# Kernel optimization log

Measured on AMD Instinct MI355X. Metric: run time of the kernel, lower is better.

Reference implementation:

```python
import jax, jax.numpy as jnp
import numpy as np

ORDER = 128


def setup_inputs() -> dict:
    key = jax.random.key(0)
    k1, k2 = jax.random.split(key)
    B, T, p, Tf = 16, 131072, ORDER, 8192
    excitation = jax.random.normal(k1, (B, T), dtype=jnp.float32)
    # reflection coefficients in (-1, 1)
    rc = jax.random.uniform(k2, (B, p, Tf), dtype=jnp.float32, minval=-1.0, maxval=1.0)
    return {"excitation": excitation, "rc": rc}


def _rc_to_lpc(rc):
    """Step-up (Levinson-Durbin) recursion: reflection coeffs -> LPC coeffs.

    rc: (B, p, T_f)  ->  a: (B, T_f, p+1) with a[..., 0] == 1.
    Each step i does a[..., 1:i+2] += k_i * flip(a[..., :i+1]).
    Implemented as a full-width masked gather so it runs in one lax.scan.
    """
    B, p, Tf = rc.shape
    ks = jnp.transpose(rc, (1, 0, 2))  # (p, B, Tf)
    a0 = jnp.zeros((B, Tf, p + 1), rc.dtype).at[..., 0].set(1.0)
    j = jnp.arange(p + 1)

    def step(a, inp):
        i, k = inp  # i: scalar order index, k: (B, Tf)
        src = jnp.clip(i + 1 - j, 0, p)
        a_rev = jnp.take(a, src, axis=-1)          # flipped prefix, full width
        mask = (j >= 1) & (j <= i + 1)             # only positions 1..i+1 update
        a = a + jnp.where(mask, k[..., None] * a_rev, jnp.zeros((), a.dtype))
        return a, None

    a, _ = jax.lax.scan(step, a0, (jnp.arange(p), ks))
    return a


def reference(excitation, rc):
    # forward: rc = rc * 0.98, then step-up recursion to LPC coefficients.
    # (the original module's FFT synthesis path is dead code and the audio
    #  passthrough is the identity; the live math is the recursion below)
    rc = rc * 0.98
    return _rc_to_lpc(rc)
```

## Files before the change

### kernel.cpp

```cpp
#include <hip/hip_runtime.h>


#define NB   16
#define ORD  128
#define TF   8192
#define PD   16

template<int M, int J>
struct PairUpd {
    static __device__ __forceinline__ void run(float (&a)[ORD + 1], float k) {
        const float lo = a[J];
        const float hi = a[M - J];
        a[J]     = fmaf(k, hi, lo);
        a[M - J] = fmaf(k, lo, hi);
        if constexpr (2 * (J + 1) < M) PairUpd<M, J + 1>::run(a, k);
    }
};

template<int M>
struct Step {
    static __device__ __forceinline__ void run(float (&a)[ORD + 1],
                                               float (&kq)[PD],
                                               const float* __restrict__ rcp) {
        constexpr int slot = (M - 1) & (PD - 1);
        const float k = 0.98f * kq[slot];
        if constexpr (M - 1 + PD < ORD)
            kq[slot] = rcp[(size_t)(M - 1 + PD) * TF];
        asm volatile("" ::: "memory");
        if constexpr (M > 2) PairUpd<M, 1>::run(a, k);
        if constexpr ((M & 1) == 0) {
            const float mid = a[M / 2];
            a[M / 2] = fmaf(k, mid, mid);
        }
        a[M] = k;
        if constexpr (M < ORD) Step<M + 1>::run(a, kq, rcp);
    }
};

template<int J>
struct Stage {
    static __device__ __forceinline__ void run(float* __restrict__ dst,
                                               const float (&a)[ORD + 1]) {
        dst[J] = a[J];
        if constexpr (J < ORD) Stage<J + 1>::run(dst, a);
    }
};

__global__ __launch_bounds__(256)
__attribute__((amdgpu_waves_per_eu(2, 2)))
void lpc_stepup_kernel(const float* __restrict__ rc, float* __restrict__ out) {
    const int tid = threadIdx.x;
    const int gid = blockIdx.x * 256 + tid;
    const int b = gid >> 13;
    const int t = gid & (TF - 1);
    const float* rcp = rc + ((size_t)b * ORD) * TF + t;

    float kq[PD];
#pragma unroll
    for (int i = 0; i < PD; ++i) kq[i] = rcp[(size_t)i * TF];

    float a[ORD + 1];
    a[0] = 1.0f;
    Step<1>::run(a, kq, rcp);

    __shared__ __align__(16) float lds[64 * (ORD + 1)];
    const int my_round = tid >> 6;
    const int row      = tid & 63;
    float* out_block = out + (size_t)blockIdx.x * 256 * (ORD + 1);

    for (int r = 0; r < 4; ++r) {
        __syncthreads();
        if (my_round == r)
            Stage<0>::run(&lds[row * (ORD + 1)], a);
        __syncthreads();
        const float4* lds4 = (const float4*)lds;
        float4* out4 = (float4*)(out_block + (size_t)r * 64 * (ORD + 1));
        for (int e = tid; e < (64 * (ORD + 1)) / 4; e += 256)
            out4[e] = lds4[e];
    }
}

extern "C" void kernel_launch(void* const* d_in, const int* in_sizes, int n_in,
                              void* d_out, int out_size, void* d_ws, size_t ws_size,
                              hipStream_t stream) {
    const float* rc = (const float*)d_in[1];
    float* out = (float*)d_out;
    dim3 grid((NB * TF) / 256);
    dim3 block(256);
    hipLaunchKernelGGL(lpc_stepup_kernel, grid, block, 0, stream, rc, out);
}
```

Before: 139.6 us.

## Use single-wave blocks and preload all reflection coefficients into registers

Each block now holds one 64-lane wave instead of four, so every wave stages its own 64 rows through LDS and writes them out without taking turns across four rounds. All 128 reflection coefficients are loaded into registers up front, replacing the rolling 16-deep prefetch queue that loaded inside the recursion. This removes the serialized staging rounds and the per-step loads, but raises register pressure (about 257 floats live) and restricts occupancy to one wave per EU, with little left to hide memory latency.

```diff
diff --git a/kernel.cpp b/kernel.cpp
--- a/kernel.cpp
+++ b/kernel.cpp
@@ -4,7 +4,6 @@
 #define NB   16
 #define ORD  128
 #define TF   8192
-#define PD   16
 
 template<int M, int J>
 struct PairUpd {
@@ -20,20 +19,15 @@
 template<int M>
 struct Step {
     static __device__ __forceinline__ void run(float (&a)[ORD + 1],
-                                               float (&kq)[PD],
-                                               const float* __restrict__ rcp) {
-        constexpr int slot = (M - 1) & (PD - 1);
-        const float k = 0.98f * kq[slot];
-        if constexpr (M - 1 + PD < ORD)
-            kq[slot] = rcp[(size_t)(M - 1 + PD) * TF];
-        asm volatile("" ::: "memory");
+                                               const float (&kq)[ORD]) {
+        const float k = 0.98f * kq[M - 1];
         if constexpr (M > 2) PairUpd<M, 1>::run(a, k);
         if constexpr ((M & 1) == 0) {
             const float mid = a[M / 2];
             a[M / 2] = fmaf(k, mid, mid);
         }
         a[M] = k;
-        if constexpr (M < ORD) Step<M + 1>::run(a, kq, rcp);
+        if constexpr (M < ORD) Step<M + 1>::run(a, kq);
     }
 };
 
@@ -46,38 +40,32 @@
     }
 };
 
-__global__ __launch_bounds__(256)
-__attribute__((amdgpu_waves_per_eu(2, 2)))
+__global__ __launch_bounds__(64)
+__attribute__((amdgpu_waves_per_eu(1, 1)))
 void lpc_stepup_kernel(const float* __restrict__ rc, float* __restrict__ out) {
-    const int tid = threadIdx.x;
-    const int gid = blockIdx.x * 256 + tid;
+    const int lane = threadIdx.x;
+    const int gid  = blockIdx.x * 64 + lane;
     const int b = gid >> 13;
     const int t = gid & (TF - 1);
     const float* rcp = rc + ((size_t)b * ORD) * TF + t;
 
-    float kq[PD];
+    float kq[ORD];
 #pragma unroll
-    for (int i = 0; i < PD; ++i) kq[i] = rcp[(size_t)i * TF];
+    for (int i = 0; i < ORD; ++i) kq[i] = rcp[(size_t)i * TF];
 
     float a[ORD + 1];
     a[0] = 1.0f;
-    Step<1>::run(a, kq, rcp);
+    Step<1>::run(a, kq);
 
     __shared__ __align__(16) float lds[64 * (ORD + 1)];
-    const int my_round = tid >> 6;
-    const int row      = tid & 63;
-    float* out_block = out + (size_t)blockIdx.x * 256 * (ORD + 1);
+    Stage<0>::run(&lds[lane * (ORD + 1)], a);
+    __syncthreads();
 
-    for (int r = 0; r < 4; ++r) {
-        __syncthreads();
-        if (my_round == r)
-            Stage<0>::run(&lds[row * (ORD + 1)], a);
-        __syncthreads();
-        const float4* lds4 = (const float4*)lds;
-        float4* out4 = (float4*)(out_block + (size_t)r * 64 * (ORD + 1));
-        for (int e = tid; e < (64 * (ORD + 1)) / 4; e += 256)
-            out4[e] = lds4[e];
-    }
+    const float4* lds4 = (const float4*)lds;
+    float4* out4 = (float4*)(out + (size_t)blockIdx.x * 64 * (ORD + 1));
+#pragma unroll 4
+    for (int e = lane; e < (64 * (ORD + 1)) / 4; e += 64)
+        out4[e] = lds4[e];
 }
 
 extern "C" void kernel_launch(void* const* d_in, const int* in_sizes, int n_in,
@@ -85,7 +73,7 @@
                               hipStream_t stream) {
     const float* rc = (const float*)d_in[1];
     float* out = (float*)d_out;
-    dim3 grid((NB * TF) / 256);
-    dim3 block(256);
+    dim3 grid((NB * TF) / 64);
+    dim3 block(64);
     hipLaunchKernelGGL(lpc_stepup_kernel, grid, block, 0, stream, rc, out);
 }
```

Result: slower. 144.2 us (+3.3%).

## Split step-up recursion into two kernels with prefix round-trip through output

Applied to the files above, without the earlier changes.

Splits the 128-step recursion into two launches. The first runs orders 1..52 and writes the partial coefficients straight to the output buffer. The second reloads them, loads the remaining reflection coefficients all up front, finishes the recursion, and writes the final rows through LDS using 128-thread blocks. This replaces the rolling 16-deep prefetch queue with fully preloaded k values in each phase, which may change register pressure and latency hiding. In exchange it adds an extra uncoalesced global write and read of 52 floats per column, plus a second launch.

```diff
diff --git a/kernel.cpp b/kernel.cpp
--- a/kernel.cpp
+++ b/kernel.cpp
@@ -1,10 +1,10 @@
 #include <hip/hip_runtime.h>
 
 
-#define NB   16
-#define ORD  128
-#define TF   8192
-#define PD   16
+#define NB    16
+#define ORD   128
+#define TF    8192
+#define SPLIT 52
 
 template<int M, int J>
 struct PairUpd {
@@ -17,23 +17,18 @@
     }
 };
 
-template<int M>
+template<int M, int MEND, int K0, int NK>
 struct Step {
     static __device__ __forceinline__ void run(float (&a)[ORD + 1],
-                                               float (&kq)[PD],
-                                               const float* __restrict__ rcp) {
-        constexpr int slot = (M - 1) & (PD - 1);
-        const float k = 0.98f * kq[slot];
-        if constexpr (M - 1 + PD < ORD)
-            kq[slot] = rcp[(size_t)(M - 1 + PD) * TF];
-        asm volatile("" ::: "memory");
+                                               const float (&kq)[NK]) {
+        const float k = 0.98f * kq[M - 1 - K0];
         if constexpr (M > 2) PairUpd<M, 1>::run(a, k);
         if constexpr ((M & 1) == 0) {
             const float mid = a[M / 2];
             a[M / 2] = fmaf(k, mid, mid);
         }
         a[M] = k;
-        if constexpr (M < ORD) Step<M + 1>::run(a, kq, rcp);
+        if constexpr (M < MEND) Step<M + 1, MEND, K0, NK>::run(a, kq);
     }
 };
 
@@ -48,34 +43,62 @@
 
 __global__ __launch_bounds__(256)
 __attribute__((amdgpu_waves_per_eu(2, 2)))
-void lpc_stepup_kernel(const float* __restrict__ rc, float* __restrict__ out) {
-    const int tid = threadIdx.x;
-    const int gid = blockIdx.x * 256 + tid;
-    const int b = gid >> 13;
-    const int t = gid & (TF - 1);
+void lpc_stepA(const float* __restrict__ rc, float* __restrict__ out) {
+    const int col = blockIdx.x * 256 + threadIdx.x;
+    const int b = col >> 13;
+    const int t = col & (TF - 1);
     const float* rcp = rc + ((size_t)b * ORD) * TF + t;
 
-    float kq[PD];
+    float kq[SPLIT];
 #pragma unroll
-    for (int i = 0; i < PD; ++i) kq[i] = rcp[(size_t)i * TF];
+    for (int i = 0; i < SPLIT; ++i) kq[i] = rcp[(size_t)i * TF];
 
     float a[ORD + 1];
     a[0] = 1.0f;
-    Step<1>::run(a, kq, rcp);
+    Step<1, SPLIT, 0, SPLIT>::run(a, kq);
+
+    float* op = out + (size_t)col * (ORD + 1);
+#pragma unroll
+    for (int j = 1; j <= SPLIT; ++j) op[j] = a[j];
+}
+
+__global__ __launch_bounds__(128)
+__attribute__((amdgpu_waves_per_eu(2, 2)))
+void lpc_stepB(const float* __restrict__ rc, float* out) {
+    const int tid = threadIdx.x;
+    const int col = blockIdx.x * 128 + tid;
+    const int b = col >> 13;
+    const int t = col & (TF - 1);
+    const float* rcp = rc + ((size_t)b * ORD) * TF + t;
+
+    constexpr int NK = ORD - SPLIT;
+    float kq[NK];
+#pragma unroll
+    for (int i = 0; i < NK; ++i) kq[i] = rcp[(size_t)(SPLIT + i) * TF];
+
+    float a[ORD + 1];
+    a[0] = 1.0f;
+    {
+        const float* op = out + (size_t)col * (ORD + 1);
+#pragma unroll
+        for (int j = 1; j <= SPLIT; ++j) a[j] = op[j];
+    }
+
+    Step<SPLIT + 1, ORD, SPLIT, NK>::run(a, kq);
 
     __shared__ __align__(16) float lds[64 * (ORD + 1)];
     const int my_round = tid >> 6;
     const int row      = tid & 63;
-    float* out_block = out + (size_t)blockIdx.x * 256 * (ORD + 1);
 
-    for (int r = 0; r < 4; ++r) {
+    for (int r = 0; r < 2; ++r) {
         __syncthreads();
         if (my_round == r)
             Stage<0>::run(&lds[row * (ORD + 1)], a);
         __syncthreads();
         const float4* lds4 = (const float4*)lds;
-        float4* out4 = (float4*)(out_block + (size_t)r * 64 * (ORD + 1));
-        for (int e = tid; e < (64 * (ORD + 1)) / 4; e += 256)
+        float4* out4 = (float4*)(out + (size_t)(blockIdx.x * 128 + r * 64) * (ORD + 1));
+#pragma unroll 4
+        for (int e = tid; e < (64 * (ORD + 1)) / 4; e += 128)
             out4[e] = lds4[e];
     }
 }
@@ -85,7 +108,6 @@
                               hipStream_t stream) {
     const float* rc = (const float*)d_in[1];
     float* out = (float*)d_out;
-    dim3 grid((NB * TF) / 256);
-    dim3 block(256);
-    hipLaunchKernelGGL(lpc_stepup_kernel, grid, block, 0, stream, rc, out);
+    hipLaunchKernelGGL(lpc_stepA, dim3((NB * TF) / 256), dim3(256), 0, stream, rc, out);
+    hipLaunchKernelGGL(lpc_stepB, dim3((NB * TF) / 128), dim3(128), 0, stream, rc, out);
 }
```

After: 173.3 us. +24.1%, slower.
